# Performance work log

Measured on AMD Instinct MI355X. Metric: run time of the kernel, lower is better.

The kernel has to match this reference:

```python
import jax, jax.numpy as jnp
import numpy as np

# 26 neighbor taps of a 3x3x3 kernel in the exact order the torch module builds them:
# raster order over (z,y,x) in {0,1,2}^3, skipping the center (1,1,1).
OFFSETS = [(i, j, k) for i in range(3) for j in range(3) for k in range(3) if (i, j, k) != (1, 1, 1)]
DILATIONS = [1, 2]


def _affinity(x, d):
    # x: [B, K, D, H, W]; conv3d(kernel, dilation=d) on replicate-padded input is
    # exactly center-minus-shifted-neighbor with edge padding.
    B, K, D, H, W = x.shape
    xp = jnp.pad(x, ((0, 0), (0, 0), (d, d), (d, d), (d, d)), mode='edge')
    diffs = [x - xp[:, :, i * d:i * d + D, j * d:j * d + H * 0 + D if False else j * d + H, k * d:k * d + W]
             for (i, j, k) in OFFSETS]
    # fix slice bounds cleanly (depth D, height H, width W)
    diffs = [x - xp[:, :, i * d:i * d + D, j * d:j * d + H, k * d:k * d + W] for (i, j, k) in OFFSETS]
    return jnp.stack(diffs, axis=2)  # [B, K, 26, D, H, W]


def setup_inputs() -> dict:
    key = jax.random.key(0)
    x = jax.random.normal(key, (1, 2, 64, 128, 128), dtype=jnp.float32)
    return {"x": x}


def reference(x):
    # out: [B, K, 26*len(DILATIONS), D, H, W]
    affs = [_affinity(x, d) for d in DILATIONS]
    return jnp.concatenate(affs, axis=2)
```

## Files before the change

kernel.cpp:

```cpp
#include <hip/hip_runtime.h>


constexpr int Kc  = 2;
constexpr int Dz  = 64;
constexpr int Hy  = 128;
constexpr int Wx  = 128;
constexpr int DHW = Dz * Hy * Wx;
constexpr int TAPS = 52;

typedef float floatx4 __attribute__((ext_vector_type(4)));

__global__ __launch_bounds__(256)
void LocalAffinity_kernel(const float* __restrict__ in, float* __restrict__ out) {
    const int tid = blockIdx.x * blockDim.x + threadIdx.x;
    const int x4 = tid & 31;
    const int y  = (tid >> 5) & 127;
    const int z  = (tid >> 12) & 63;
    const int kk = tid >> 18;
    const int x0 = x4 << 2;

    const float* __restrict__ base = in + kk * DHW;
    const float* crow = base + (z * Hy + y) * Wx + x0;
    const float c0 = crow[0], c1 = crow[1], c2 = crow[2], c3 = crow[3];

    float* obase = out + (size_t)kk * ((size_t)TAPS * DHW) + (size_t)(z * Hy + y) * Wx + x0;

    #pragma unroll
    for (int t = 0; t < TAPS; ++t) {
        const int d   = (t < 26) ? 1 : 2;
        const int tt  = (t < 26) ? t : t - 26;
        const int idx = (tt < 13) ? tt : tt + 1;
        const int di  = idx / 9 - 1;
        const int dj  = (idx / 3) % 3 - 1;
        const int dk  = idx % 3 - 1;

        const int zc = min(max(z + di * d, 0), Dz - 1);
        const int yc = min(max(y + dj * d, 0), Hy - 1);
        const float* row = base + (zc * Hy + yc) * Wx;

        const int xb = x0 + dk * d;
        const int xa0 = min(max(xb + 0, 0), Wx - 1);
        const int xa1 = min(max(xb + 1, 0), Wx - 1);
        const int xa2 = min(max(xb + 2, 0), Wx - 1);
        const int xa3 = min(max(xb + 3, 0), Wx - 1);

        floatx4 o;
        o.x = c0 - row[xa0];
        o.y = c1 - row[xa1];
        o.z = c2 - row[xa2];
        o.w = c3 - row[xa3];

        __builtin_nontemporal_store(o, (floatx4*)(obase + (size_t)t * DHW));
    }
}

extern "C" void kernel_launch(void* const* d_in, const int* in_sizes, int n_in,
                              void* d_out, int out_size, void* d_ws, size_t ws_size,
                              hipStream_t stream) {
    const float* x = (const float*)d_in[0];
    float* out = (float*)d_out;
    const int total = Kc * Dz * Hy * (Wx / 4);
    const int block = 256;
    const int grid = total / block;
    LocalAffinity_kernel<<<grid, block, 0, stream>>>(x, out);
}
```

Baseline: 448.1 us.

## Load neighbor rows as float4 once and shift x-taps via lane shuffles

Each thread now loads one aligned float4 per (dz,dy) neighbor row and builds the three x-shifted variants with cross-lane shuffles, replacing the per-tap scalar clamped gathers. Edge replication at the row ends uses the thread's own values. Blocks are remapped so consecutive block IDs are spread across depth slabs and channels, which changes how concurrently running blocks touch memory. The kernel is dominated by output stores, so fewer loads may change little, and the shuffles add some instruction overhead.

```diff
diff --git a/kernel.cpp b/kernel.cpp
--- a/kernel.cpp
+++ b/kernel.cpp
@@ -1,7 +1,6 @@
 #include <hip/hip_runtime.h>
 
 
-constexpr int Kc  = 2;
 constexpr int Dz  = 64;
 constexpr int Hy  = 128;
 constexpr int Wx  = 128;
@@ -10,47 +9,81 @@
 
 typedef float floatx4 __attribute__((ext_vector_type(4)));
 
+__device__ __forceinline__ int iclamp(int v, int hi) { return v < 0 ? 0 : (v > hi ? hi : v); }
+
 __global__ __launch_bounds__(256)
 void LocalAffinity_kernel(const float* __restrict__ in, float* __restrict__ out) {
-    const int tid = blockIdx.x * blockDim.x + threadIdx.x;
-    const int x4 = tid & 31;
-    const int y  = (tid >> 5) & 127;
-    const int z  = (tid >> 12) & 63;
-    const int kk = tid >> 18;
-    const int x0 = x4 << 2;
+    const int b    = blockIdx.x;
+    const int slab = b & 15;
+    const int w    = b >> 4;
+    const int kk   = slab >> 3;
+    const int z    = ((slab & 7) << 3) | (w >> 4);
+    const int idx  = ((w & 15) << 8) | threadIdx.x;
+    const int y    = idx >> 5;
+    const int x4   = idx & 31;
+    const int x0   = x4 << 2;
 
     const float* __restrict__ base = in + kk * DHW;
-    const float* crow = base + (z * Hy + y) * Wx + x0;
-    const float c0 = crow[0], c1 = crow[1], c2 = crow[2], c3 = crow[3];
+    const floatx4 c = *(const floatx4*)(base + (z * Hy + y) * Wx + x0);
 
-    float* obase = out + (size_t)kk * ((size_t)TAPS * DHW) + (size_t)(z * Hy + y) * Wx + x0;
+    float* obase = out + (size_t)kk * ((size_t)TAPS * DHW) + (size_t)((z * Hy + y) * Wx + x0);
 
     #pragma unroll
-    for (int t = 0; t < TAPS; ++t) {
-        const int d   = (t < 26) ? 1 : 2;
-        const int tt  = (t < 26) ? t : t - 26;
-        const int idx = (tt < 13) ? tt : tt + 1;
-        const int di  = idx / 9 - 1;
-        const int dj  = (idx / 3) % 3 - 1;
-        const int dk  = idx % 3 - 1;
+    for (int dd = 1; dd <= 2; ++dd) {
+        #pragma unroll
+        for (int di = -1; di <= 1; ++di) {
+            #pragma unroll
+            for (int dj = -1; dj <= 1; ++dj) {
+                floatx4 v;
+                if (di == 0 && dj == 0) {
+                    v = c;
+                } else {
+                    const int zc = iclamp(z + di * dd, Dz - 1);
+                    const int yc = iclamp(y + dj * dd, Hy - 1);
+                    v = *(const floatx4*)(base + (zc * Hy + yc) * Wx + x0);
+                }
+                #pragma unroll
+                for (int dk = -1; dk <= 1; ++dk) {
+                    if (di == 0 && dj == 0 && dk == 0) continue;
+                    const int raster = (di + 1) * 9 + (dj + 1) * 3 + (dk + 1);
+                    const int t26    = raster < 13 ? raster : raster - 1;
+                    const int t      = t26 + (dd == 1 ? 0 : 26);
 
-        const int zc = min(max(z + di * d, 0), Dz - 1);
-        const int yc = min(max(y + dj * d, 0), Hy - 1);
-        const float* row = base + (zc * Hy + yc) * Wx;
+                    floatx4 s;
+                    if (dk == 0) {
+                        s = v;
+                    } else if (dk < 0) {
+                        if (dd == 1) {
+                            float sm = __shfl_up(v.w, 1);
+                            sm = (x4 == 0) ? v.x : sm;
+                            s.x = sm; s.y = v.x; s.z = v.y; s.w = v.z;
+                        } else {
+                            float a  = __shfl_up(v.z, 1);
+                            float bb = __shfl_up(v.w, 1);
+                            a  = (x4 == 0) ? v.x : a;
+                            bb = (x4 == 0) ? v.x : bb;
+                            s.x = a; s.y = bb; s.z = v.x; s.w = v.y;
+                        }
+                    } else {
+                        if (dd == 1) {
+                            float sp = __shfl_down(v.x, 1);
+                            sp = (x4 == 31) ? v.w : sp;
+                            s.x = v.y; s.y = v.z; s.z = v.w; s.w = sp;
+                        } else {
+                            float a  = __shfl_down(v.x, 1);
+                            float bb = __shfl_down(v.y, 1);
+                            a  = (x4 == 31) ? v.w : a;
+                            bb = (x4 == 31) ? v.w : bb;
+                            s.x = v.z; s.y = v.w; s.z = a; s.w = bb;
+                        }
+                    }
 
-        const int xb = x0 + dk * d;
-        const int xa0 = min(max(xb + 0, 0), Wx - 1);
-        const int xa1 = min(max(xb + 1, 0), Wx - 1);
-        const int xa2 = min(max(xb + 2, 0), Wx - 1);
-        const int xa3 = min(max(xb + 3, 0), Wx - 1);
-
-        floatx4 o;
-        o.x = c0 - row[xa0];
-        o.y = c1 - row[xa1];
-        o.z = c2 - row[xa2];
-        o.w = c3 - row[xa3];
-
-        __builtin_nontemporal_store(o, (floatx4*)(obase + (size_t)t * DHW));
+                    floatx4 o;
+                    o.x = c.x - s.x; o.y = c.y - s.y; o.z = c.z - s.z; o.w = c.w - s.w;
+                    __builtin_nontemporal_store(o, (floatx4*)(obase + (size_t)t * DHW));
+                }
+            }
+        }
     }
 }
 
@@ -59,8 +92,5 @@
                               hipStream_t stream) {
     const float* x = (const float*)d_in[0];
     float* out = (float*)d_out;
-    const int total = Kc * Dz * Hy * (Wx / 4);
-    const int block = 256;
-    const int grid = total / block;
-    LocalAffinity_kernel<<<grid, block, 0, stream>>>(x, out);
+    LocalAffinity_kernel<<<2048, 256, 0, stream>>>(x, out);
 }
```

Result: faster. 429.7 us (-4.1%).
